# Optimization experiments

Hardware: AMD Instinct MI355X
Metric: run time of the kernel (lower is better)

The kernel has to match this reference:

```python
import jax, jax.numpy as jnp
import numpy as np

B, N = 1, 512
C_S, C_Z, C_H, H, PQ, PV = 384, 128, 16, 12, 4, 8
INF, EPS = 1e5, 1e-8
HW_INIT = 0.541324854612918  # softplus^{-1}(1), ipa_point_weights_init_


def _rotary(t, rot_dim, theta=10000.0):
    # lucidrains interleaved rotary over residue axis (axis 1); rotates first rot_dim channels
    n = t.shape[1]
    inv_freq = 1.0 / (theta ** (jnp.arange(0, rot_dim, 2, dtype=jnp.float32) / rot_dim))
    freqs = jnp.arange(n, dtype=jnp.float32)[:, None] * inv_freq  # [N, rot_dim//2]
    cos = jnp.cos(freqs)[None, :, None, :].astype(t.dtype)
    sin = jnp.sin(freqs)[None, :, None, :].astype(t.dtype)
    tr, tp = t[..., :rot_dim], t[..., rot_dim:]
    x1, x2 = tr[..., 0::2], tr[..., 1::2]
    tr = jnp.stack([x1 * cos - x2 * sin, x1 * sin + x2 * cos], axis=-1).reshape(tr.shape)
    return jnp.concatenate([tr, tp], axis=-1)


def _ipa(s, z, rot, trans, mask, Wq, bq, Wkv, bkv, Wqp, bqp, Wkvp, bkvp, Wb, bb,
         head_weights, Whid, bhid, Wpair, bpair, Wpts, bpts, Wpn, bpn):
    Bx, Nx = s.shape[0], s.shape[1]
    q = (s @ Wq + bq).reshape(Bx, Nx, H, C_H)
    kv = (s @ Wkv + bkv).reshape(Bx, Nx, H, 2 * C_H)
    k, v = kv[..., :C_H], kv[..., C_H:]

    def make_pts(x, npts):
        # channel layout: [x-block, y-block, z-block] -> [B,N,H*npts,3], then rigid apply R@p+t
        x = jnp.stack(jnp.split(x, 3, axis=-1), axis=-1)
        x = jnp.einsum('bnij,bnpj->bnpi', rot, x) + trans[:, :, None, :]
        return x.reshape(Bx, Nx, H, npts, 3)

    q_pts = make_pts(s @ Wqp + bqp, PQ)
    kv_pts = make_pts(s @ Wkvp + bkvp, PQ + PV)
    k_pts, v_pts = kv_pts[..., :PQ, :], kv_pts[..., PQ:, :]

    q = _rotary(q, C_H // 2)
    k = _rotary(k, C_H // 2)

    a = jnp.einsum('bihc,bjhc->bhij', q, k) * np.sqrt(1.0 / (3 * C_H))
    a = a + np.sqrt(1.0 / 3.0) * (jnp.einsum('bijc,ch->bhij', z, Wb) + bb[None, :, None, None])
    d2 = jnp.sum((q_pts[:, :, None] - k_pts[:, None]) ** 2, axis=-1)  # [B,Ni,Nj,H,PQ]
    hw = jax.nn.softplus(head_weights) * np.sqrt(1.0 / (3 * (PQ * 9.0 / 2)))
    a = a + jnp.transpose(-0.5 * jnp.sum(d2 * hw[None, None, None, :, None], axis=-1), (0, 3, 1, 2))
    sq_mask = INF * (mask[:, :, None] * mask[:, None, :] - 1.0)
    a = jax.nn.softmax(a + sq_mask[:, None], axis=-1)  # [B,H,N,N]

    o = jnp.einsum('bhij,bjhc->bihc', a, v).reshape(Bx, Nx, H * C_H)
    o_pt = jnp.einsum('bhij,bjhpx->bihpx', a, v_pts)  # [B,N,H,PV,3]
    o_pt = jnp.einsum('bnji,bnhpj->bnhpi', rot, o_pt - trans[:, :, None, None, :])  # invert_apply
    o_pt_norm = jnp.sqrt(jnp.sum(o_pt ** 2, axis=-1) + EPS).reshape(Bx, Nx, H * PV)
    o_pt = o_pt.reshape(Bx, Nx, H * PV, 3)
    pts_feat = jnp.concatenate([o_pt[..., 0], o_pt[..., 1], o_pt[..., 2]], axis=-1)
    o_pair = jnp.einsum('bhij,bijc->bihc', a, z).reshape(Bx, Nx, H * C_Z)

    s_out = ((o @ Whid + bhid) + (o_pair @ Wpair + bpair)
             + (pts_feat @ Wpts + bpts) + (o_pt_norm @ Wpn + bpn))
    return s_out, a


def setup_inputs() -> dict:
    key = jax.random.key(0)
    ks = jax.random.split(key, 16)
    f = lambda i, shape: jax.random.normal(ks[i], shape, dtype=jnp.float32)
    sc = 0.02
    rot, _ = jnp.linalg.qr(f(2, (B, N, 3, 3)))
    return {
        's': f(0, (B, N, C_S)),
        'z': f(1, (B, N, N, C_Z)),
        'rot': rot,
        'trans': f(3, (B, N, 3)),
        'mask': jnp.ones((B, N), jnp.float32),
        'Wq': f(4, (C_S, H * C_H)) * sc, 'bq': jnp.zeros((H * C_H,), jnp.float32),
        'Wkv': f(5, (C_S, 2 * H * C_H)) * sc, 'bkv': jnp.zeros((2 * H * C_H,), jnp.float32),
        'Wqp': f(6, (C_S, H * PQ * 3)) * sc, 'bqp': jnp.zeros((H * PQ * 3,), jnp.float32),
        'Wkvp': f(7, (C_S, H * (PQ + PV) * 3)) * sc, 'bkvp': jnp.zeros((H * (PQ + PV) * 3,), jnp.float32),
        'Wb': f(8, (C_Z, H)) * sc, 'bb': jnp.zeros((H,), jnp.float32),
        'head_weights': jnp.full((H,), HW_INIT, jnp.float32),
        'Whid': f(9, (H * C_H, C_S)) * sc, 'bhid': jnp.zeros((C_S,), jnp.float32),
        'Wpair': f(10, (H * C_Z, C_S)) * sc, 'bpair': jnp.zeros((C_S,), jnp.float32),
        'Wpts': f(11, (H * PV * 3, C_S)) * sc, 'bpts': jnp.zeros((C_S,), jnp.float32),
        'Wpn': f(12, (H * PV, C_S)) * sc, 'bpn': jnp.zeros((C_S,), jnp.float32),
    }


def reference(s, z, rot, trans, mask, Wq, bq, Wkv, bkv, Wqp, bqp, Wkvp, bkvp, Wb, bb,
              head_weights, Whid, bhid, Wpair, bpair, Wpts, bpts, Wpn, bpn):
    return _ipa(s, z, rot, trans, mask, Wq, bq, Wkv, bkv, Wqp, bqp, Wkvp, bkvp, Wb, bb,
                head_weights, Whid, bhid, Wpair, bpair, Wpts, bpts, Wpn, bpn)
```

## Files before the change

### kernel.cpp

```cpp
#include <hip/hip_runtime.h>
#include <hip/hip_bf16.h>
#include <cmath>

#define N 512
#define C_S 384
#define C_Z 128
#define C_H 16
#define H 12
#define PQ 4
#define PV 8

#define NJC 4
#define JCHUNK (N / NJC)
#define NPART 2016
#define NFEAT 2112
#define NRAW 1152
#define KSPLIT 11
#define KCHUNK 192

#define WS_Q    0
#define WS_K    (WS_Q + N*H*C_H)
#define WS_V    (WS_K + N*H*C_H)
#define WS_QP   (WS_V + N*H*C_H)
#define WS_KP   (WS_QP + N*H*PQ*3)
#define WS_VP   (WS_KP + N*H*PQ*3)
#define WS_PART (WS_VP + N*H*PV*3)
#define WS_FEAT (WS_PART + N*NJC*NPART)
#define WS_RAW  WS_PART
#define WS_KT   (WS_PART + 1200000)
#define WS_KPT  (WS_KT + 98304)
#define WS_WBT  (WS_KPT + 73728)
#define WS_FOUT WS_PART

__global__ __launch_bounds__(256) void k_gemm_proj(
    const float* __restrict__ s,
    const float* __restrict__ Wq,  const float* __restrict__ bq,
    const float* __restrict__ Wkv, const float* __restrict__ bkv,
    const float* __restrict__ Wqp, const float* __restrict__ bqp,
    const float* __restrict__ Wkvp,const float* __restrict__ bkvp,
    float* __restrict__ raw_out)
{
    const int m0 = blockIdx.x * 64;
    const int c0 = blockIdx.y * 64;
    const int t  = threadIdx.x;
    const int tc = t & 15;
    const int tm = t >> 4;

    __shared__ float st[64 * 33];
    __shared__ float wt[32 * 64];

    float acc[4][4];
#pragma unroll
    for (int u = 0; u < 4; ++u) {
        int col = c0 + tc*4 + u;
        const float* b; int cb;
        if (col < 192)      { b = bq;   cb = 0; }
        else if (col < 576) { b = bkv;  cb = 192; }
        else if (col < 720) { b = bqp;  cb = 576; }
        else                { b = bkvp; cb = 720; }
        float bv = b[col - cb];
#pragma unroll
        for (int r = 0; r < 4; ++r) acc[r][u] = bv;
    }

    for (int k0 = 0; k0 < C_S; k0 += 32) {
        __syncthreads();
        for (int e = t; e < 512; e += 256) {
            int row = e >> 3, kq = e & 7;
            float4 v = *(const float4*)&s[(size_t)(m0 + row)*C_S + k0 + kq*4];
            st[row*33 + kq*4 + 0] = v.x;
            st[row*33 + kq*4 + 1] = v.y;
            st[row*33 + kq*4 + 2] = v.z;
            st[row*33 + kq*4 + 3] = v.w;
        }
        for (int e = t; e < 512; e += 256) {
            int kk = e >> 4, c4 = e & 15;
            int col = c0 + c4*4;
            const float* W; int ncol, cb;
            if (col < 192)      { W = Wq;   ncol = 192; cb = 0; }
            else if (col < 576) { W = Wkv;  ncol = 384; cb = 192; }
            else if (col < 720) { W = Wqp;  ncol = 144; cb = 576; }
            else                { W = Wkvp; ncol = 432; cb = 720; }
            float4 v = *(const float4*)&W[(size_t)(k0 + kk)*ncol + (col - cb)];
            *(float4*)&wt[kk*64 + c4*4] = v;
        }
        __syncthreads();

#pragma unroll 8
        for (int kk = 0; kk < 32; ++kk) {
            float4 w = *(const float4*)&wt[kk*64 + tc*4];
            float sv[4];
#pragma unroll
            for (int r = 0; r < 4; ++r) sv[r] = st[(tm*4 + r)*33 + kk];
#pragma unroll
            for (int r = 0; r < 4; ++r) {
                acc[r][0] += sv[r] * w.x;
                acc[r][1] += sv[r] * w.y;
                acc[r][2] += sv[r] * w.z;
                acc[r][3] += sv[r] * w.w;
            }
        }
    }

#pragma unroll
    for (int r = 0; r < 4; ++r) {
        float4 o = make_float4(acc[r][0], acc[r][1], acc[r][2], acc[r][3]);
        *(float4*)&raw_out[(size_t)(m0 + tm*4 + r)*NRAW + c0 + tc*4] = o;
    }
}

__global__ __launch_bounds__(256) void k_post(
    const float* __restrict__ raw_in, const float* __restrict__ rot,
    const float* __restrict__ trans, const float* __restrict__ Wb,
    float* __restrict__ ws)
{
    const int n = blockIdx.x;
    const int t = threadIdx.x;
    __shared__ float raw[NRAW];

    for (int idx = t; idx < NRAW; idx += 256) raw[idx] = raw_in[(size_t)n*NRAW + idx];
    __syncthreads();

    if (n == 0) {
        for (int idx = t; idx < H*C_Z; idx += 256) {
            int h = idx >> 7, c = idx & 127;
            ws[WS_WBT + h*128 + c] = Wb[c*H + h];
        }
    }

    float R[9], T[3];
#pragma unroll
    for (int u = 0; u < 9; ++u) R[u] = rot[n*9 + u];
#pragma unroll
    for (int u = 0; u < 3; ++u) T[u] = trans[n*3 + u];

    float* q   = ws + WS_Q;
    float* v   = ws + WS_V;
    float* qp  = ws + WS_QP;
    float* vp  = ws + WS_VP;
    float* kT  = ws + WS_KT;
    float* kpT = ws + WS_KPT;

    for (int idx = t; idx < 1152; idx += 256) {
        if (idx < 192) {
            int h = idx >> 4, c = idx & 15;
            float val;
            if (c < 8) {
                int f = c >> 1;
                float x1 = raw[h*16 + 2*f];
                float x2 = raw[h*16 + 2*f + 1];
                float ang = (float)n * powf(10000.0f, -(float)(2*f) / 8.0f);
                float cs = cosf(ang), sn = sinf(ang);
                val = (c & 1) ? (x1*sn + x2*cs) : (x1*cs - x2*sn);
            } else {
                val = raw[h*16 + c];
            }
            q[n*192 + idx] = val;
        } else if (idx < 384) {
            int o = idx - 192, h = o >> 4, c = o & 15;
            float val;
            if (c < 8) {
                int f = c >> 1;
                float x1 = raw[192 + h*32 + 2*f];
                float x2 = raw[192 + h*32 + 2*f + 1];
                float ang = (float)n * powf(10000.0f, -(float)(2*f) / 8.0f);
                float cs = cosf(ang), sn = sinf(ang);
                val = (c & 1) ? (x1*sn + x2*cs) : (x1*cs - x2*sn);
            } else {
                val = raw[192 + h*32 + c];
            }
            kT[(size_t)o*N + n] = val;
        } else if (idx < 576) {
            int o = idx - 384, h = o >> 4, c = o & 15;
            v[n*192 + o] = raw[192 + h*32 + 16 + c];
        } else if (idx < 720) {
            int o = idx - 576;
            int hp = o / 3, ic = o - hp*3;
            float acc = T[ic];
#pragma unroll
            for (int j = 0; j < 3; ++j) acc += R[ic*3 + j] * raw[576 + j*48 + hp];
            qp[n*144 + o] = acc;
        } else {
            int o = idx - 720;
            int hp = o / 3, ic = o - hp*3;
            int h = hp / 12, p = hp - h*12;
            float acc = T[ic];
#pragma unroll
            for (int j = 0; j < 3; ++j) acc += R[ic*3 + j] * raw[720 + j*144 + hp];
            if (p < PQ) kpT[(size_t)(h*12 + p*3 + ic)*N + n] = acc;
            else        vp[n*(H*PV*3) + (h*PV + (p - PQ))*3 + ic] = acc;
        }
    }
}

__global__ __launch_bounds__(512) void k_logits(
    const float* __restrict__ ws, const float* __restrict__ z,
    const float* __restrict__ bb,
    const float* __restrict__ hwts, const float* __restrict__ mask,
    float* __restrict__ a_out)
{
    const int i  = blockIdx.x;
    const int j0 = blockIdx.y * 128;
    const int t  = threadIdx.x;
    const int l  = t & 63;
    const int w  = t >> 6;
    const int jh = w >> 2;
    const int h0 = __builtin_amdgcn_readfirstlane(3 * (w & 3));
    const int j  = l + 64*jh;
    const int jg = j0 + j;

    __shared__ float zt[128*132];

    for (int e = t; e < 4096; e += 512) {
        int row = e >> 5, cq = e & 31;
        float4 v4 = *(const float4*)&z[(((size_t)i*N) + j0 + row)*C_Z + cq*4];
        *(float4*)&zt[row*132 + cq*4] = v4;
    }
    __syncthreads();

    const float* q   = ws + WS_Q  + (size_t)i*192;
    const float* qp  = ws + WS_QP + (size_t)i*144;
    const float* kT  = ws + WS_KT;
    const float* kpT = ws + WS_KPT;

    const float c1 = sqrtf(1.0f / 48.0f);
    const float c2 = sqrtf(1.0f / 3.0f);
    const float mterm = 100000.0f * (mask[i] * mask[jg] - 1.0f);

    float qkd[3];
#pragma unroll
    for (int u = 0; u < 3; ++u) {
        const int h = h0 + u;
        float qk = 0.0f;
#pragma unroll
        for (int c = 0; c < 16; ++c)
            qk += q[h*16 + c] * kT[(size_t)(h*16 + c)*N + jg];
        float d2s = 0.0f;
#pragma unroll
        for (int e = 0; e < 12; ++e) {
            float d = qp[h*12 + e] - kpT[(size_t)(h*12 + e)*N + jg];
            d2s += d*d;
        }
        float hw = log1pf(expf(hwts[h])) * sqrtf(1.0f / 54.0f);
        qkd[u] = c1*qk - 0.5f*hw*d2s + mterm + c2*bb[h];
    }

    const float* w0 = ws + WS_WBT + (size_t)h0*128;
    float acc[3] = {0.0f, 0.0f, 0.0f};
#pragma unroll 8
    for (int c4 = 0; c4 < 32; ++c4) {
        float4 zv = *(const float4*)&zt[j*132 + c4*4];
        float4 b0 = *(const float4*)&w0[c4*4];
        float4 b1 = *(const float4*)&w0[128 + c4*4];
        float4 b2 = *(const float4*)&w0[256 + c4*4];
        acc[0] += zv.x*b0.x + zv.y*b0.y + zv.z*b0.z + zv.w*b0.w;
        acc[1] += zv.x*b1.x + zv.y*b1.y + zv.z*b1.z + zv.w*b1.w;
        acc[2] += zv.x*b2.x + zv.y*b2.y + zv.z*b2.z + zv.w*b2.w;
    }

#pragma unroll
    for (int u = 0; u < 3; ++u)
        a_out[((size_t)(h0 + u)*N + i)*N + jg] = qkd[u] + c2*acc[u];
}

__global__ __launch_bounds__(256) void k_softmax(float* __restrict__ a)
{
    const int row  = blockIdx.x*4 + (threadIdx.x >> 6);
    const int lane = threadIdx.x & 63;
    float* r = a + (size_t)row * N;

    float v[8];
    float m = -1e30f;
#pragma unroll
    for (int u = 0; u < 8; ++u) { v[u] = r[lane + 64*u]; m = fmaxf(m, v[u]); }
#pragma unroll
    for (int off = 32; off; off >>= 1) m = fmaxf(m, __shfl_xor(m, off));
    float ssum = 0.0f;
#pragma unroll
    for (int u = 0; u < 8; ++u) { v[u] = expf(v[u] - m); ssum += v[u]; }
#pragma unroll
    for (int off = 32; off; off >>= 1) ssum += __shfl_xor(ssum, off);
    float inv = 1.0f / ssum;
#pragma unroll
    for (int u = 0; u < 8; ++u) r[lane + 64*u] = v[u] * inv;
}

__global__ __launch_bounds__(256) void k_av(
    const float* __restrict__ a_full, const float* __restrict__ ws_ro,
    const float* __restrict__ z, float* __restrict__ ws)
{
    const int i  = blockIdx.x;
    const int jc = blockIdx.y;
    const int j0 = jc * JCHUNK;
    const int t  = threadIdx.x;

    __shared__ float a_s[H*JCHUNK];

    const float* v  = ws_ro + WS_V;
    const float* vp = ws_ro + WS_VP;
    float* part = ws + WS_PART + ((size_t)i*NJC + jc)*NPART;

    for (int e = t; e < H*JCHUNK; e += 256) {
        int h = e >> 7, jj = e & (JCHUNK-1);
        a_s[e] = a_full[((size_t)h*N + i)*N + j0 + jj];
    }
    __syncthreads();

    for (int idx = t; idx < 480; idx += 256) {
        float acc = 0.0f;
        if (idx < 192) {
            int h = idx >> 4;
            const float* vv = v + (size_t)j0*192 + idx;
            const float* ar = &a_s[h*JCHUNK];
#pragma unroll 8
            for (int jj = 0; jj < JCHUNK; ++jj) acc += ar[jj] * vv[(size_t)jj*192];
        } else {
            int o = idx - 192;
            int h = (o/3) >> 3;
            const float* vv = vp + (size_t)j0*288 + o;
            const float* ar = &a_s[h*JCHUNK];
#pragma unroll 8
            for (int jj = 0; jj < JCHUNK; ++jj) acc += ar[jj] * vv[(size_t)jj*288];
        }
        part[idx] = acc;
    }

    {
        const int c  = t & 127;
        const int hb = t >> 7;
        float acc[6];
#pragma unroll
        for (int u = 0; u < 6; ++u) acc[u] = 0.0f;
        const float* zi = z + ((size_t)i*N + j0)*C_Z + c;
        for (int jj = 0; jj < JCHUNK; jj += 8) {
            float zr[8];
#pragma unroll
            for (int r = 0; r < 8; ++r) zr[r] = zi[(size_t)(jj+r)*C_Z];
            float4 av0[6], av1[6];
#pragma unroll
            for (int u = 0; u < 6; ++u) {
                av0[u] = *(const float4*)&a_s[(hb + 2*u)*JCHUNK + jj];
                av1[u] = *(const float4*)&a_s[(hb + 2*u)*JCHUNK + jj + 4];
            }
#pragma unroll
            for (int u = 0; u < 6; ++u) {
                acc[u] += av0[u].x*zr[0] + av0[u].y*zr[1] + av0[u].z*zr[2] + av0[u].w*zr[3];
                acc[u] += av1[u].x*zr[4] + av1[u].y*zr[5] + av1[u].z*zr[6] + av1[u].w*zr[7];
            }
        }
#pragma unroll
        for (int u = 0; u < 6; ++u) part[480 + (hb + 2*u)*C_Z + c] = acc[u];
    }
}

__global__ __launch_bounds__(256) void k_feat(
    const float* __restrict__ rot, const float* __restrict__ trans,
    float* __restrict__ ws)
{
    const int i = blockIdx.x;
    const int t = threadIdx.x;

    __shared__ float vec[NPART];

    const float* part = ws + WS_PART + (size_t)i*NJC*NPART;
    float* feat = ws + WS_FEAT + (size_t)i*NFEAT;

    for (int e = t; e < NPART; e += 256) {
        float acc = 0.0f;
#pragma unroll
        for (int jc = 0; jc < NJC; ++jc) acc += part[(size_t)jc*NPART + e];
        vec[e] = acc;
    }
    __syncthreads();

    for (int e = t; e < NPART; e += 256) {
        if (e < 192)       feat[e] = vec[e];
        else if (e >= 480) feat[192 + (e - 480)] = vec[e];
    }

    if (t < H*PV) {
        const int hp = t;
        float T0 = trans[i*3+0], T1 = trans[i*3+1], T2 = trans[i*3+2];
        float px = vec[192 + hp*3 + 0] - T0;
        float py = vec[192 + hp*3 + 1] - T1;
        float pz = vec[192 + hp*3 + 2] - T2;
        const float* R = rot + i*9;
        float ox = R[0]*px + R[3]*py + R[6]*pz;
        float oy = R[1]*px + R[4]*py + R[7]*pz;
        float oz = R[2]*px + R[5]*py + R[8]*pz;
        feat[1728 + hp]       = ox;
        feat[1728 + 96 + hp]  = oy;
        feat[1728 + 192 + hp] = oz;
        feat[2016 + hp] = sqrtf(ox*ox + oy*oy + oz*oz + 1e-8f);
    }
}

__global__ __launch_bounds__(256) void k_final_part(
    const float* __restrict__ ws,
    const float* __restrict__ Whid, const float* __restrict__ Wpair,
    const float* __restrict__ Wpts, const float* __restrict__ Wpn,
    float* __restrict__ fout)
{
    const int m0 = blockIdx.x * 64;
    const int c0 = blockIdx.y * 64;
    const int kc = blockIdx.z;
    const int t  = threadIdx.x;
    const int tc = t & 15;
    const int tm = t >> 4;

    __shared__ float ft[64 * 33];
    __shared__ float wt[32 * 64];

    const float* feat = ws + WS_FEAT;

    float acc[4][4];
#pragma unroll
    for (int r = 0; r < 4; ++r)
#pragma unroll
        for (int u = 0; u < 4; ++u) acc[r][u] = 0.0f;

    const int kbase = kc * KCHUNK;
    for (int k0 = kbase; k0 < kbase + KCHUNK; k0 += 32) {
        const float* W; int r0;
        if (k0 < 192)       { W = Whid;  r0 = k0; }
        else if (k0 < 1728) { W = Wpair; r0 = k0 - 192; }
        else if (k0 < 2016) { W = Wpts;  r0 = k0 - 1728; }
        else                { W = Wpn;   r0 = k0 - 2016; }

        __syncthreads();
        for (int e = t; e < 512; e += 256) {
            int row = e >> 3, kq = e & 7;
            float4 v = *(const float4*)&feat[(size_t)(m0 + row)*NFEAT + k0 + kq*4];
            ft[row*33 + kq*4 + 0] = v.x;
            ft[row*33 + kq*4 + 1] = v.y;
            ft[row*33 + kq*4 + 2] = v.z;
            ft[row*33 + kq*4 + 3] = v.w;
        }
        for (int e = t; e < 512; e += 256) {
            int kk = e >> 4, c4 = e & 15;
            float4 v = *(const float4*)&W[(size_t)(r0 + kk)*C_S + c0 + c4*4];
            *(float4*)&wt[kk*64 + c4*4] = v;
        }
        __syncthreads();

#pragma unroll 8
        for (int kk = 0; kk < 32; ++kk) {
            float4 w = *(const float4*)&wt[kk*64 + tc*4];
            float sv[4];
#pragma unroll
            for (int r = 0; r < 4; ++r) sv[r] = ft[(tm*4 + r)*33 + kk];
#pragma unroll
            for (int r = 0; r < 4; ++r) {
                acc[r][0] += sv[r] * w.x;
                acc[r][1] += sv[r] * w.y;
                acc[r][2] += sv[r] * w.z;
                acc[r][3] += sv[r] * w.w;
            }
        }
    }

#pragma unroll
    for (int r = 0; r < 4; ++r) {
        float4 o = make_float4(acc[r][0], acc[r][1], acc[r][2], acc[r][3]);
        *(float4*)&fout[((size_t)kc*N + m0 + tm*4 + r)*C_S + c0 + tc*4] = o;
    }
}

__global__ __launch_bounds__(256) void k_red(
    const float* __restrict__ fout,
    const float* __restrict__ bhid, const float* __restrict__ bpair,
    const float* __restrict__ bpts, const float* __restrict__ bpn,
    float* __restrict__ s_out)
{
    const int idx = blockIdx.x * 256 + threadIdx.x;
    const int c = idx % C_S;
    float acc = bhid[c] + bpair[c] + bpts[c] + bpn[c];
#pragma unroll
    for (int kc = 0; kc < KSPLIT; ++kc)
        acc += fout[(size_t)kc*N*C_S + idx];
    s_out[idx] = acc;
}

extern "C" void kernel_launch(void* const* d_in, const int* in_sizes, int n_in,
                              void* d_out, int out_size, void* d_ws, size_t ws_size,
                              hipStream_t stream) {
    const float* s     = (const float*)d_in[0];
    const float* z     = (const float*)d_in[1];
    const float* rot   = (const float*)d_in[2];
    const float* trans = (const float*)d_in[3];
    const float* mask  = (const float*)d_in[4];
    const float* Wq    = (const float*)d_in[5];
    const float* bq    = (const float*)d_in[6];
    const float* Wkv   = (const float*)d_in[7];
    const float* bkv   = (const float*)d_in[8];
    const float* Wqp   = (const float*)d_in[9];
    const float* bqp   = (const float*)d_in[10];
    const float* Wkvp  = (const float*)d_in[11];
    const float* bkvp  = (const float*)d_in[12];
    const float* Wb    = (const float*)d_in[13];
    const float* bb    = (const float*)d_in[14];
    const float* hwts  = (const float*)d_in[15];
    const float* Whid  = (const float*)d_in[16];
    const float* bhid  = (const float*)d_in[17];
    const float* Wpair = (const float*)d_in[18];
    const float* bpair = (const float*)d_in[19];
    const float* Wpts  = (const float*)d_in[20];
    const float* bpts  = (const float*)d_in[21];
    const float* Wpn   = (const float*)d_in[22];
    const float* bpn   = (const float*)d_in[23];

    float* out   = (float*)d_out;
    float* s_out = out;
    float* a_out = out + N*C_S;
    float* ws    = (float*)d_ws;

    k_gemm_proj<<<dim3(8, 18), 256, 0, stream>>>(s, Wq, bq, Wkv, bkv, Wqp, bqp,
                                                 Wkvp, bkvp, ws + WS_RAW);
    k_post<<<N, 256, 0, stream>>>(ws + WS_RAW, rot, trans, Wb, ws);
    k_logits<<<dim3(N, 4), 512, 0, stream>>>(ws, z, bb, hwts, mask, a_out);
    k_softmax<<<(H*N)/4, 256, 0, stream>>>(a_out);
    k_av<<<dim3(N, NJC), 256, 0, stream>>>(a_out, ws, z, ws);
    k_feat<<<N, 256, 0, stream>>>(rot, trans, ws);
    k_final_part<<<dim3(8, 6, KSPLIT), 256, 0, stream>>>(ws, Whid, Wpair, Wpts,
                                                         Wpn, ws + WS_FOUT);
    k_red<<<(N*C_S)/256, 256, 0, stream>>>(ws + WS_FOUT, bhid, bpair, bpts, bpn,
                                           s_out);
}
```

Measured before the change: 179.1 us.

## Prefetch z tile into registers and overlap with logits compute in smaller blocks

The logits kernel now uses 256-thread blocks covering 64 columns instead of 512-thread blocks covering 128, halving shared memory per block. The z tile is loaded from global memory into registers at kernel start, so the load latency overlaps the q·k and point-distance computation. The tile is then staged into shared memory in two halves, with a barrier between them. This trades extra synchronisations and register pressure for better latency hiding and occupancy.

```diff
diff --git a/kernel.cpp b/kernel.cpp
--- a/kernel.cpp
+++ b/kernel.cpp
@@ -193,30 +193,39 @@
     }
 }
 
-__global__ __launch_bounds__(512) void k_logits(
+__global__ __launch_bounds__(256) void k_logits(
     const float* __restrict__ ws, const float* __restrict__ z,
     const float* __restrict__ bb,
     const float* __restrict__ hwts, const float* __restrict__ mask,
     float* __restrict__ a_out)
 {
     const int i  = blockIdx.x;
-    const int j0 = blockIdx.y * 128;
+    const int j0 = blockIdx.y * 64;
     const int t  = threadIdx.x;
-    const int l  = t & 63;
-    const int w  = t >> 6;
-    const int jh = w >> 2;
-    const int h0 = __builtin_amdgcn_readfirstlane(3 * (w & 3));
-    const int j  = l + 64*jh;
+    const int j  = t & 63;
     const int jg = j0 + j;
-
-    __shared__ float zt[128*132];
-
-    for (int e = t; e < 4096; e += 512) {
-        int row = e >> 5, cq = e & 31;
-        float4 v4 = *(const float4*)&z[(((size_t)i*N) + j0 + row)*C_Z + cq*4];
-        *(float4*)&zt[row*132 + cq*4] = v4;
-    }
-    __syncthreads();
+    const int h0 = __builtin_amdgcn_readfirstlane(3 * (t >> 6));
+
+    __shared__ float zt[64*132];
+
+    const int srow = t >> 2;
+    const int scq  = t & 3;
+    float4 ra0, ra1, ra2, ra3, rb0, rb1, rb2, rb3;
+    {
+        const float* zbase = z + (((size_t)i*N) + j0)*C_Z;
+        int e0 = t,       r0_ = e0 >> 4, c0_ = e0 & 15;
+        int e1 = t + 256, r1_ = e1 >> 4, c1_ = e1 & 15;
+        int e2 = t + 512, r2_ = e2 >> 4, c2_ = e2 & 15;
+        int e3 = t + 768, r3_ = e3 >> 4, c3_ = e3 & 15;
+        ra0 = *(const float4*)&zbase[(size_t)r0_*C_Z + c0_*4];
+        ra1 = *(const float4*)&zbase[(size_t)r1_*C_Z + c1_*4];
+        ra2 = *(const float4*)&zbase[(size_t)r2_*C_Z + c2_*4];
+        ra3 = *(const float4*)&zbase[(size_t)r3_*C_Z + c3_*4];
+        rb0 = *(const float4*)&zbase[(size_t)r0_*C_Z + 64 + c0_*4];
+        rb1 = *(const float4*)&zbase[(size_t)r1_*C_Z + 64 + c1_*4];
+        rb2 = *(const float4*)&zbase[(size_t)r2_*C_Z + 64 + c2_*4];
+        rb3 = *(const float4*)&zbase[(size_t)r3_*C_Z + 64 + c3_*4];
+    }
 
     const float* q   = ws + WS_Q  + (size_t)i*192;
     const float* qp  = ws + WS_QP + (size_t)i*144;
@@ -245,10 +254,46 @@
         qkd[u] = c1*qk - 0.5f*hw*d2s + mterm + c2*bb[h];
     }
 
+    {
+        int e0 = t,       r0_ = e0 >> 4, c0_ = e0 & 15;
+        int e1 = t + 256, r1_ = e1 >> 4, c1_ = e1 & 15;
+        int e2 = t + 512, r2_ = e2 >> 4, c2_ = e2 & 15;
+        int e3 = t + 768, r3_ = e3 >> 4, c3_ = e3 & 15;
+        *(float4*)&zt[r0_*132 + c0_*4] = ra0;
+        *(float4*)&zt[r1_*132 + c1_*4] = ra1;
+        *(float4*)&zt[r2_*132 + c2_*4] = ra2;
+        *(float4*)&zt[r3_*132 + c3_*4] = ra3;
+    }
+    __syncthreads();
+
     const float* w0 = ws + WS_WBT + (size_t)h0*128;
     float acc[3] = {0.0f, 0.0f, 0.0f};
-#pragma unroll 8
-    for (int c4 = 0; c4 < 32; ++c4) {
+#pragma unroll
+    for (int c4 = 0; c4 < 16; ++c4) {
+        float4 zv = *(const float4*)&zt[j*132 + c4*4];
+        float4 b0 = *(const float4*)&w0[c4*4];
+        float4 b1 = *(const float4*)&w0[128 + c4*4];
+        float4 b2 = *(const float4*)&w0[256 + c4*4];
+        acc[0] += zv.x*b0.x + zv.y*b0.y + zv.z*b0.z + zv.w*b0.w;
+        acc[1] += zv.x*b1.x + zv.y*b1.y + zv.z*b1.z + zv.w*b1.w;
+        acc[2] += zv.x*b2.x + zv.y*b2.y + zv.z*b2.z + zv.w*b2.w;
+    }
+    __syncthreads();
+
+    {
+        int e0 = t,       r0_ = e0 >> 4, c0_ = e0 & 15;
+        int e1 = t + 256, r1_ = e1 >> 4, c1_ = e1 & 15;
+        int e2 = t + 512, r2_ = e2 >> 4, c2_ = e2 & 15;
+        int e3 = t + 768, r3_ = e3 >> 4, c3_ = e3 & 15;
+        *(float4*)&zt[r0_*132 + 64 + c0_*4] = rb0;
+        *(float4*)&zt[r1_*132 + 64 + c1_*4] = rb1;
+        *(float4*)&zt[r2_*132 + 64 + c2_*4] = rb2;
+        *(float4*)&zt[r3_*132 + 64 + c3_*4] = rb3;
+    }
+    __syncthreads();
+
+#pragma unroll
+    for (int c4 = 16; c4 < 32; ++c4) {
         float4 zv = *(const float4*)&zt[j*132 + c4*4];
         float4 b0 = *(const float4*)&w0[c4*4];
         float4 b1 = *(const float4*)&w0[128 + c4*4];
@@ -517,7 +562,7 @@
     k_gemm_proj<<<dim3(8, 18), 256, 0, stream>>>(s, Wq, bq, Wkv, bkv, Wqp, bqp,
                                                  Wkvp, bkvp, ws + WS_RAW);
     k_post<<<N, 256, 0, stream>>>(ws + WS_RAW, rot, trans, Wb, ws);
-    k_logits<<<dim3(N, 4), 512, 0, stream>>>(ws, z, bb, hwts, mask, a_out);
+    k_logits<<<dim3(N, 8), 256, 0, stream>>>(ws, z, bb, hwts, mask, a_out);
     k_softmax<<<(H*N)/4, 256, 0, stream>>>(a_out);
     k_av<<<dim3(N, NJC), 256, 0, stream>>>(a_out, ws, z, ws);
     k_feat<<<N, 256, 0, stream>>>(rot, trans, ws);
```

Result: faster. 164.1 us (-8.4%).
